# Optimization experiments

Measured on AMD Instinct MI355X. Metric: run time of the kernel, lower is better.

## Reference

```python
import jax, jax.numpy as jnp
import numpy as np

B, T_HIST, D, H = 32768, 50, 3, 512
FUTURE = 30


def gru_cell(x, h, W_ih, W_hh, b_ih, b_hh):
    # PyTorch GRU cell math: gates ordered (r, z, n)
    gi = x @ W_ih.T + b_ih          # [B, 3H]
    gh = h @ W_hh.T + b_hh          # [B, 3H]
    i_r, i_z, i_n = jnp.split(gi, 3, axis=-1)
    h_r, h_z, h_n = jnp.split(gh, 3, axis=-1)
    r = jax.nn.sigmoid(i_r + h_r)
    z = jax.nn.sigmoid(i_z + h_z)
    n = jnp.tanh(i_n + r * h_n)
    return (1.0 - z) * n + z * h


def setup_inputs() -> dict:
    key = jax.random.key(0)
    ks = jax.random.split(key, 20)
    s = 0.04  # ~1/sqrt(H), matches PyTorch uniform init scale
    def p(k, shape):
        return jax.random.normal(k, shape, dtype=jnp.float32) * s
    return {
        "x_input": jax.random.normal(ks[0], (B, T_HIST, D), dtype=jnp.float32),
        "future_len": FUTURE,
        # encoder GRU, layer 0 (input D) and layer 1 (input H)
        "enc_W_ih0": p(ks[1], (3 * H, D)), "enc_W_hh0": p(ks[2], (3 * H, H)),
        "enc_b_ih0": p(ks[3], (3 * H,)),  "enc_b_hh0": p(ks[4], (3 * H,)),
        "enc_W_ih1": p(ks[5], (3 * H, H)), "enc_W_hh1": p(ks[6], (3 * H, H)),
        "enc_b_ih1": p(ks[7], (3 * H,)),  "enc_b_hh1": p(ks[8], (3 * H,)),
        # decoder GRU, layer 0 (input D = output_dim) and layer 1
        "dec_W_ih0": p(ks[9], (3 * H, D)), "dec_W_hh0": p(ks[10], (3 * H, H)),
        "dec_b_ih0": p(ks[11], (3 * H,)), "dec_b_hh0": p(ks[12], (3 * H,)),
        "dec_W_ih1": p(ks[13], (3 * H, H)), "dec_W_hh1": p(ks[14], (3 * H, H)),
        "dec_b_ih1": p(ks[15], (3 * H,)), "dec_b_hh1": p(ks[16], (3 * H,)),
        # output projection
        "fc_W": p(ks[17], (D, H)), "fc_b": p(ks[18], (D,)),
    }


def reference(x_input, future_len,
              enc_W_ih0, enc_W_hh0, enc_b_ih0, enc_b_hh0,
              enc_W_ih1, enc_W_hh1, enc_b_ih1, enc_b_hh1,
              dec_W_ih0, dec_W_hh0, dec_b_ih0, dec_b_hh0,
              dec_W_ih1, dec_W_hh1, dec_b_ih1, dec_b_hh1,
              fc_W, fc_b):
    b = x_input.shape[0]
    h_init = jnp.zeros((b, H), dtype=x_input.dtype)

    # ---- encoder: 2-layer GRU over history (eval mode, no dropout) ----
    def enc_step(carry, x_t):
        h0, h1 = carry
        h0 = gru_cell(x_t, h0, enc_W_ih0, enc_W_hh0, enc_b_ih0, enc_b_hh0)
        h1 = gru_cell(h0, h1, enc_W_ih1, enc_W_hh1, enc_b_ih1, enc_b_hh1)
        return (h0, h1), None

    (h0, h1), _ = jax.lax.scan(enc_step, (h_init, h_init),
                               jnp.swapaxes(x_input, 0, 1))  # [T, B, D]

    def dec_step(carry, _):
        d0, d1, xin = carry
        d0 = gru_cell(xin, d0, dec_W_ih0, dec_W_hh0, dec_b_ih0, dec_b_hh0)
        d1 = gru_cell(d0, d1, dec_W_ih1, dec_W_hh1, dec_b_ih1, dec_b_hh1)
        pred = d1 @ fc_W.T + fc_b  # [B, D]
        return (d0, d1, pred), pred

    _, outs = jax.lax.scan(dec_step, (h0, h1, x_input[:, -1, :]),
                           None, length=future_len)  # [F, B, D]
    return jnp.swapaxes(outs, 0, 1)  # [B, F, D]
```

## Files before the change

kernel.cpp:

```cpp
#include <hip/hip_runtime.h>
#include <hip/hip_fp16.h>
#include <stdint.h>

typedef _Float16 h8 __attribute__((ext_vector_type(8)));
typedef float f4 __attribute__((ext_vector_type(4)));

#define DEV static __device__ __forceinline__

constexpr int BATCH  = 32768;
constexpr int HID    = 512;
constexpr int T_HIST = 50;
constexpr int FUT    = 30;
constexpr int BM = 128, BN = 32, BK = 64;

DEV void gl2lds16(const void* g, void* l) {
  __builtin_amdgcn_global_load_lds(
      (const __attribute__((address_space(1))) void*)g,
      (__attribute__((address_space(3))) void*)l,
      16, 0, 0);
}

DEV float sigm(float x)     { return 1.f / (1.f + __expf(-x)); }
DEV float tanhfast(float x) { return 1.f - 2.f / (__expf(2.f * x) + 1.f); }

__global__ void zero_fill(float4* __restrict__ p, int n4) {
  int i = blockIdx.x * 256 + threadIdx.x;
  if (i < n4) p[i] = float4{0.f, 0.f, 0.f, 0.f};
}

__global__ void pack_w(const float* __restrict__ Wa, const float* __restrict__ Wb,
                       _Float16* __restrict__ out, int KC) {
  int i = blockIdx.x * 256 + threadIdx.x;
  int total = 16 * KC * 3 * 32 * 64;
  if (i >= total) return;
  int k0  = i & 7;
  int k8s = (i >> 3) & 7;
  int n   = (i >> 6) & 31;
  int t   = i >> 11;
  int g   = t % 3;
  int t2  = t / 3;
  int kc  = t2 % KC;
  int nb  = t2 / KC;
  int k8  = k8s ^ (n & 7);
  int row = g * 512 + nb * 32 + n;
  int kg  = kc * 64 + k8 * 8 + k0;
  float v = (kg < 512) ? Wa[(size_t)row * 512 + kg] : Wb[(size_t)row * 512 + kg - 512];
  out[i] = (_Float16)v;
}

__global__ void pack_bias(const float* __restrict__ bih, const float* __restrict__ bhh,
                          float* __restrict__ out) {
  int j = blockIdx.x * 256 + threadIdx.x;
  if (j >= 512) return;
  out[j]        = bih[j]        + bhh[j];
  out[512 + j]  = bih[512 + j]  + bhh[512 + j];
  out[1024 + j] = bih[1024 + j];
  out[1536 + j] = bhh[1024 + j];
}

__global__ void pack_wx(const float* __restrict__ Wih, float* __restrict__ out) {
  int i = blockIdx.x * 256 + threadIdx.x;
  if (i >= 512 * 9) return;
  int j = i / 9, q = i % 9, g = q / 3, k = q % 3;
  out[i] = Wih[(size_t)(g * 512 + j) * 3 + k];
}

template <int KC, bool L0>
__launch_bounds__(256, 3)
__global__ void gru_step(const _Float16* __restrict__ Bp,
                         const _Float16* __restrict__ Alo,
                         const _Float16* __restrict__ Ahi,
                         _Float16* __restrict__ hnew16,
                         const float* __restrict__ bias,
                         const float* __restrict__ Wx,
                         const float* __restrict__ xin,
                         int xstride) {
  __shared__ alignas(16) _Float16 sA[BM * BK];
  __shared__ alignas(16) _Float16 sB[3 * BN * BK];

  const int tid  = threadIdx.x;
  const int wave = tid >> 6;
  const int lane = tid & 63;
  const int quad = lane >> 4;
  const int l15  = lane & 15;
  const int L  = blockIdx.x;
  const int c  = L & 7;
  const int q  = L >> 3;
  const int cb = q & 15;
  const int rb = (c << 5) | (q >> 4);
  const int row0 = rb * BM;
  const int col0 = cb * BN;

  f4 acc_r[2][2]  = {};
  f4 acc_z[2][2]  = {};
  f4 acc_n0[2][2] = {};
  f4 acc_n1[2][2] = {};

  const _Float16* Bblk = Bp + (size_t)cb * KC * (3 * BN * BK);

  for (int kc = 0; kc < KC; ++kc) {
    const _Float16* Asrc = (KC == 16 && kc >= 8) ? Ahi : Alo;
    const int kb = (kc & 7) * BK;
#pragma unroll
    for (int i = 0; i < 4; ++i) {
      int ga = wave * 256 + i * 64 + lane;
      int m = ga >> 3, k8s = ga & 7;
      int k8l = k8s ^ (m & 7);
      gl2lds16(Asrc + (size_t)(row0 + m) * HID + kb + k8l * 8,
               &sA[(wave * 256 + i * 64) * 8]);
    }
    const _Float16* Bsrc = Bblk + (size_t)kc * (3 * BN * BK);
#pragma unroll
    for (int i = 0; i < 3; ++i) {
      int gb = wave * 192 + i * 64 + lane;
      gl2lds16(Bsrc + (size_t)gb * 8, &sB[(wave * 192 + i * 64) * 8]);
    }
    __syncthreads();
#pragma unroll
    for (int s = 0; s < 2; ++s) {
      const int sw = ((s * 4 + quad) ^ (l15 & 7)) * 8;
      h8 af[2];
#pragma unroll
      for (int mt = 0; mt < 2; ++mt)
        af[mt] = *(const h8*)&sA[(wave * 32 + mt * 16 + l15) * BK + sw];
#pragma unroll
      for (int nt = 0; nt < 2; ++nt) {
        const int nrow = nt * 16 + l15;
        h8 br = *(const h8*)&sB[(0 * BN + nrow) * BK + sw];
        h8 bz = *(const h8*)&sB[(1 * BN + nrow) * BK + sw];
        h8 bn = *(const h8*)&sB[(2 * BN + nrow) * BK + sw];
#pragma unroll
        for (int mt = 0; mt < 2; ++mt) {
          acc_r[mt][nt] = __builtin_amdgcn_mfma_f32_16x16x32_f16(af[mt], br, acc_r[mt][nt], 0, 0, 0);
          acc_z[mt][nt] = __builtin_amdgcn_mfma_f32_16x16x32_f16(af[mt], bz, acc_z[mt][nt], 0, 0, 0);
          if (L0 || kc >= 8)
            acc_n1[mt][nt] = __builtin_amdgcn_mfma_f32_16x16x32_f16(af[mt], bn, acc_n1[mt][nt], 0, 0, 0);
          else
            acc_n0[mt][nt] = __builtin_amdgcn_mfma_f32_16x16x32_f16(af[mt], bn, acc_n0[mt][nt], 0, 0, 0);
        }
      }
    }
    __syncthreads();
  }

  const _Float16* hold16 = L0 ? Alo : Ahi;
  float bR[2], bZ[2], bI[2], bH[2];
  float wx[2][9];
#pragma unroll
  for (int nt = 0; nt < 2; ++nt) {
    int j = col0 + nt * 16 + l15;
    bR[nt] = bias[j];
    bZ[nt] = bias[512 + j];
    bI[nt] = bias[1024 + j];
    bH[nt] = bias[1536 + j];
    if constexpr (L0) {
#pragma unroll
      for (int q2 = 0; q2 < 9; ++q2) wx[nt][q2] = Wx[j * 9 + q2];
    }
  }
  float xv[2][4][3];
  if constexpr (L0) {
#pragma unroll
    for (int mt = 0; mt < 2; ++mt)
#pragma unroll
      for (int r = 0; r < 4; ++r) {
        int b = row0 + wave * 32 + mt * 16 + quad * 4 + r;
        const float* xp = xin + (size_t)b * xstride;
        xv[mt][r][0] = xp[0]; xv[mt][r][1] = xp[1]; xv[mt][r][2] = xp[2];
      }
  }
#pragma unroll
  for (int mt = 0; mt < 2; ++mt) {
#pragma unroll
    for (int r = 0; r < 4; ++r) {
      int b = row0 + wave * 32 + mt * 16 + quad * 4 + r;
#pragma unroll
      for (int nt = 0; nt < 2; ++nt) {
        int j = col0 + nt * 16 + l15;
        size_t idx = (size_t)b * HID + j;
        float rr = acc_r[mt][nt][r] + bR[nt];
        float zz = acc_z[mt][nt][r] + bZ[nt];
        float hn = acc_n1[mt][nt][r] + bH[nt];
        float in_;
        if constexpr (L0) {
          const float* w = wx[nt];
          rr += xv[mt][r][0] * w[0] + xv[mt][r][1] * w[1] + xv[mt][r][2] * w[2];
          zz += xv[mt][r][0] * w[3] + xv[mt][r][1] * w[4] + xv[mt][r][2] * w[5];
          in_ = bI[nt] + xv[mt][r][0] * w[6] + xv[mt][r][1] * w[7] + xv[mt][r][2] * w[8];
        } else {
          in_ = acc_n0[mt][nt][r] + bI[nt];
        }
        float rg = sigm(rr);
        float zg = sigm(zz);
        float ng = tanhfast(in_ + rg * hn);
        float hp = (float)hold16[idx];
        float hv = (1.f - zg) * ng + zg * hp;
        hnew16[idx] = (_Float16)hv;
      }
    }
  }
}

__global__ __launch_bounds__(256) void fc_kernel(const _Float16* __restrict__ h,
                                                 const float* __restrict__ W,
                                                 const float* __restrict__ bfc,
                                                 float* __restrict__ out) {
  int wave = threadIdx.x >> 6, lane = threadIdx.x & 63;
  int b = blockIdx.x * 4 + wave;
  const h8* hp = (const h8*)(h + (size_t)b * 512);
  h8 a0 = hp[lane];
  float s[3];
#pragma unroll
  for (int d = 0; d < 3; ++d) {
    const float4* wp = (const float4*)(W + d * 512);
    float4 w0 = wp[lane * 2], w1 = wp[lane * 2 + 1];
    s[d] = (float)a0[0] * w0.x + (float)a0[1] * w0.y + (float)a0[2] * w0.z + (float)a0[3] * w0.w
         + (float)a0[4] * w1.x + (float)a0[5] * w1.y + (float)a0[6] * w1.z + (float)a0[7] * w1.w;
  }
#pragma unroll
  for (int d = 0; d < 3; ++d)
#pragma unroll
    for (int off = 32; off > 0; off >>= 1) s[d] += __shfl_xor(s[d], off, 64);
  if (lane == 0) {
    out[(size_t)b * 90 + 0] = s[0] + bfc[0];
    out[(size_t)b * 90 + 1] = s[1] + bfc[1];
    out[(size_t)b * 90 + 2] = s[2] + bfc[2];
  }
}

extern "C" void kernel_launch(void* const* d_in, const int* in_sizes, int n_in,
                              void* d_out, int out_size, void* d_ws, size_t ws_size,
                              hipStream_t stream) {
  (void)in_sizes; (void)n_in; (void)out_size; (void)ws_size;
  const float* x_input = (const float*)d_in[0];
  const float* eWih0 = (const float*)d_in[2];
  const float* eWhh0 = (const float*)d_in[3];
  const float* ebih0 = (const float*)d_in[4];
  const float* ebhh0 = (const float*)d_in[5];
  const float* eWih1 = (const float*)d_in[6];
  const float* eWhh1 = (const float*)d_in[7];
  const float* ebih1 = (const float*)d_in[8];
  const float* ebhh1 = (const float*)d_in[9];
  const float* dWih0 = (const float*)d_in[10];
  const float* dWhh0 = (const float*)d_in[11];
  const float* dbih0 = (const float*)d_in[12];
  const float* dbhh0 = (const float*)d_in[13];
  const float* dWih1 = (const float*)d_in[14];
  const float* dWhh1 = (const float*)d_in[15];
  const float* dbih1 = (const float*)d_in[16];
  const float* dbhh1 = (const float*)d_in[17];
  const float* fcW   = (const float*)d_in[18];
  const float* fcb   = (const float*)d_in[19];
  float* out = (float*)d_out;

  char* ws = (char*)d_ws;
  const size_t S16 = (size_t)BATCH * HID * 2;
  _Float16* h0h[2] = {(_Float16*)(ws),            (_Float16*)(ws + S16)};
  _Float16* h1h[2] = {(_Float16*)(ws + 2 * S16),  (_Float16*)(ws + 3 * S16)};
  char* p = ws + 4 * S16;
  const size_t W8  = (size_t)16 * 8  * 3 * 32 * 64 * 2;
  const size_t W16 = (size_t)16 * 16 * 3 * 32 * 64 * 2;
  _Float16* pkE0 = (_Float16*)p; p += W8;
  _Float16* pkE1 = (_Float16*)p; p += W16;
  _Float16* pkD0 = (_Float16*)p; p += W8;
  _Float16* pkD1 = (_Float16*)p; p += W16;
  float* bE0 = (float*)p; p += 2048 * 4;
  float* bE1 = (float*)p; p += 2048 * 4;
  float* bD0 = (float*)p; p += 2048 * 4;
  float* bD1 = (float*)p; p += 2048 * 4;
  float* wxE = (float*)p; p += 512 * 9 * 4;
  float* wxD = (float*)p; p += 512 * 9 * 4;

  pack_w<<<dim3(3072), 256, 0, stream>>>(eWhh0, eWhh0, pkE0, 8);
  pack_w<<<dim3(6144), 256, 0, stream>>>(eWih1, eWhh1, pkE1, 16);
  pack_w<<<dim3(3072), 256, 0, stream>>>(dWhh0, dWhh0, pkD0, 8);
  pack_w<<<dim3(6144), 256, 0, stream>>>(dWih1, dWhh1, pkD1, 16);
  pack_bias<<<2, 256, 0, stream>>>(ebih0, ebhh0, bE0);
  pack_bias<<<2, 256, 0, stream>>>(ebih1, ebhh1, bE1);
  pack_bias<<<2, 256, 0, stream>>>(dbih0, dbhh0, bD0);
  pack_bias<<<2, 256, 0, stream>>>(dbih1, dbhh1, bD1);
  pack_wx<<<18, 256, 0, stream>>>(eWih0, wxE);
  pack_wx<<<18, 256, 0, stream>>>(dWih0, wxD);

  {
    int n4 = (int)(S16 / 16);
    zero_fill<<<(n4 + 255) / 256, 256, 0, stream>>>((float4*)h0h[0], n4);
    zero_fill<<<(n4 + 255) / 256, 256, 0, stream>>>((float4*)h1h[0], n4);
  }

  dim3 grid(4096), blk(256);
  int p0 = 0, p1 = 0;
  for (int t = 0; t < T_HIST; ++t) {
    gru_step<8, true><<<grid, blk, 0, stream>>>(pkE0, h0h[p0], nullptr,
                                                h0h[1 - p0], bE0, wxE,
                                                x_input + (size_t)t * 3, 150);
    p0 ^= 1;
    gru_step<16, false><<<grid, blk, 0, stream>>>(pkE1, h0h[p0], h1h[p1],
                                                  h1h[1 - p1], bE1, nullptr, nullptr, 0);
    p1 ^= 1;
  }
  for (int t = 0; t < FUT; ++t) {
    const float* xp; int xs;
    if (t == 0) { xp = x_input + (size_t)49 * 3; xs = 150; }
    else        { xp = out + (size_t)(t - 1) * 3; xs = 90; }
    gru_step<8, true><<<grid, blk, 0, stream>>>(pkD0, h0h[p0], nullptr,
                                                h0h[1 - p0], bD0, wxD, xp, xs);
    p0 ^= 1;
    gru_step<16, false><<<grid, blk, 0, stream>>>(pkD1, h0h[p0], h1h[p1],
                                                  h1h[1 - p1], bD1, nullptr, nullptr, 0);
    p1 ^= 1;
    fc_kernel<<<8192, 256, 0, stream>>>(h1h[p1], fcW, fcb, out + (size_t)t * 3);
  }
}
```

Measured before the change: 15.57 ms.

## Load A fragments directly from global memory and double K chunk size

The activation (A) tile is no longer staged through LDS. Each lane now reads its MFMA fragments straight from global memory into registers. The K chunk grows from 64 to 128, so the weight tile in LDS doubles and the packed weight layout and swizzle are redone for 16 groups of 8 halves. This halves the number of K iterations and barriers and frees the LDS the A tile used, but A reads become uncoalesced 16-byte loads issued inside the MFMA loop with no prefetch.

```diff
diff --git a/kernel.cpp b/kernel.cpp
--- a/kernel.cpp
+++ b/kernel.cpp
@@ -11,7 +11,7 @@
 constexpr int HID    = 512;
 constexpr int T_HIST = 50;
 constexpr int FUT    = 30;
-constexpr int BM = 128, BN = 32, BK = 64;
+constexpr int BM = 128, BN = 32, BK = 128;
 
 DEV void gl2lds16(const void* g, void* l) {
   __builtin_amdgcn_global_load_lds(
@@ -29,21 +29,21 @@
 }
 
 __global__ void pack_w(const float* __restrict__ Wa, const float* __restrict__ Wb,
-                       _Float16* __restrict__ out, int KC) {
+                       _Float16* __restrict__ out, int KCC) {
   int i = blockIdx.x * 256 + threadIdx.x;
-  int total = 16 * KC * 3 * 32 * 64;
+  int total = 16 * KCC * 3 * 32 * 128;
   if (i >= total) return;
-  int k0  = i & 7;
-  int k8s = (i >> 3) & 7;
-  int n   = (i >> 6) & 31;
-  int t   = i >> 11;
-  int g   = t % 3;
-  int t2  = t / 3;
-  int kc  = t2 % KC;
-  int nb  = t2 / KC;
-  int k8  = k8s ^ (n & 7);
-  int row = g * 512 + nb * 32 + n;
-  int kg  = kc * 64 + k8 * 8 + k0;
+  int k0   = i & 7;
+  int g16s = (i >> 3) & 15;
+  int n    = (i >> 7) & 31;
+  int t    = i >> 12;
+  int g    = t % 3;
+  int t2   = t / 3;
+  int kc   = t2 % KCC;
+  int nb   = t2 / KCC;
+  int g16  = g16s ^ (n & 15);
+  int row  = g * 512 + nb * 32 + n;
+  int kg   = kc * 128 + g16 * 8 + k0;
   float v = (kg < 512) ? Wa[(size_t)row * 512 + kg] : Wb[(size_t)row * 512 + kg - 512];
   out[i] = (_Float16)v;
 }
@@ -65,7 +65,7 @@
   out[i] = Wih[(size_t)(g * 512 + j) * 3 + k];
 }
 
-template <int KC, bool L0>
+template <int KCC, bool L0>
 __launch_bounds__(256, 3)
 __global__ void gru_step(const _Float16* __restrict__ Bp,
                          const _Float16* __restrict__ Alo,
@@ -75,7 +75,6 @@
                          const float* __restrict__ Wx,
                          const float* __restrict__ xin,
                          int xstride) {
-  __shared__ alignas(16) _Float16 sA[BM * BK];
   __shared__ alignas(16) _Float16 sB[3 * BN * BK];
 
   const int tid  = threadIdx.x;
@@ -96,44 +95,37 @@
   f4 acc_n0[2][2] = {};
   f4 acc_n1[2][2] = {};
 
-  const _Float16* Bblk = Bp + (size_t)cb * KC * (3 * BN * BK);
-
-  for (int kc = 0; kc < KC; ++kc) {
-    const _Float16* Asrc = (KC == 16 && kc >= 8) ? Ahi : Alo;
-    const int kb = (kc & 7) * BK;
-#pragma unroll
-    for (int i = 0; i < 4; ++i) {
-      int ga = wave * 256 + i * 64 + lane;
-      int m = ga >> 3, k8s = ga & 7;
-      int k8l = k8s ^ (m & 7);
-      gl2lds16(Asrc + (size_t)(row0 + m) * HID + kb + k8l * 8,
-               &sA[(wave * 256 + i * 64) * 8]);
-    }
+  const _Float16* Bblk = Bp + (size_t)cb * KCC * (3 * BN * BK);
+  const size_t aoff0 = (size_t)(row0 + wave * 32 + l15) * HID + quad * 8;
+  const size_t aoff1 = aoff0 + (size_t)16 * HID;
+
+  for (int kc = 0; kc < KCC; ++kc) {
+    const _Float16* Asrc = (KCC == 8 && kc >= 4) ? Ahi : Alo;
+    const int kb = (kc & 3) * BK;
     const _Float16* Bsrc = Bblk + (size_t)kc * (3 * BN * BK);
 #pragma unroll
-    for (int i = 0; i < 3; ++i) {
-      int gb = wave * 192 + i * 64 + lane;
-      gl2lds16(Bsrc + (size_t)gb * 8, &sB[(wave * 192 + i * 64) * 8]);
+    for (int i = 0; i < 6; ++i) {
+      int gb = wave * 384 + i * 64 + lane;
+      gl2lds16(Bsrc + (size_t)gb * 8, &sB[(wave * 384 + i * 64) * 8]);
     }
     __syncthreads();
 #pragma unroll
-    for (int s = 0; s < 2; ++s) {
-      const int sw = ((s * 4 + quad) ^ (l15 & 7)) * 8;
+    for (int s = 0; s < 4; ++s) {
       h8 af[2];
-#pragma unroll
-      for (int mt = 0; mt < 2; ++mt)
-        af[mt] = *(const h8*)&sA[(wave * 32 + mt * 16 + l15) * BK + sw];
+      af[0] = *(const h8*)&Asrc[aoff0 + kb + s * 32];
+      af[1] = *(const h8*)&Asrc[aoff1 + kb + s * 32];
+      const int g16s = (s * 4 + quad) ^ l15;
 #pragma unroll
       for (int nt = 0; nt < 2; ++nt) {
         const int nrow = nt * 16 + l15;
-        h8 br = *(const h8*)&sB[(0 * BN + nrow) * BK + sw];
-        h8 bz = *(const h8*)&sB[(1 * BN + nrow) * BK + sw];
-        h8 bn = *(const h8*)&sB[(2 * BN + nrow) * BK + sw];
+        h8 br = *(const h8*)&sB[((0 * BN + nrow) * 16 + g16s) * 8];
+        h8 bz = *(const h8*)&sB[((1 * BN + nrow) * 16 + g16s) * 8];
+        h8 bn = *(const h8*)&sB[((2 * BN + nrow) * 16 + g16s) * 8];
 #pragma unroll
         for (int mt = 0; mt < 2; ++mt) {
           acc_r[mt][nt] = __builtin_amdgcn_mfma_f32_16x16x32_f16(af[mt], br, acc_r[mt][nt], 0, 0, 0);
           acc_z[mt][nt] = __builtin_amdgcn_mfma_f32_16x16x32_f16(af[mt], bz, acc_z[mt][nt], 0, 0, 0);
-          if (L0 || kc >= 8)
+          if (L0 || kc >= 4)
             acc_n1[mt][nt] = __builtin_amdgcn_mfma_f32_16x16x32_f16(af[mt], bn, acc_n1[mt][nt], 0, 0, 0);
           else
             acc_n0[mt][nt] = __builtin_amdgcn_mfma_f32_16x16x32_f16(af[mt], bn, acc_n0[mt][nt], 0, 0, 0);
@@ -258,12 +250,12 @@
   _Float16* h0h[2] = {(_Float16*)(ws),            (_Float16*)(ws + S16)};
   _Float16* h1h[2] = {(_Float16*)(ws + 2 * S16),  (_Float16*)(ws + 3 * S16)};
   char* p = ws + 4 * S16;
-  const size_t W8  = (size_t)16 * 8  * 3 * 32 * 64 * 2;
-  const size_t W16 = (size_t)16 * 16 * 3 * 32 * 64 * 2;
-  _Float16* pkE0 = (_Float16*)p; p += W8;
-  _Float16* pkE1 = (_Float16*)p; p += W16;
-  _Float16* pkD0 = (_Float16*)p; p += W8;
-  _Float16* pkD1 = (_Float16*)p; p += W16;
+  const size_t W4 = (size_t)16 * 4 * 3 * 32 * 128 * 2;
+  const size_t W8 = (size_t)16 * 8 * 3 * 32 * 128 * 2;
+  _Float16* pkE0 = (_Float16*)p; p += W4;
+  _Float16* pkE1 = (_Float16*)p; p += W8;
+  _Float16* pkD0 = (_Float16*)p; p += W4;
+  _Float16* pkD1 = (_Float16*)p; p += W8;
   float* bE0 = (float*)p; p += 2048 * 4;
   float* bE1 = (float*)p; p += 2048 * 4;
   float* bD0 = (float*)p; p += 2048 * 4;
@@ -271,10 +263,10 @@
   float* wxE = (float*)p; p += 512 * 9 * 4;
   float* wxD = (float*)p; p += 512 * 9 * 4;
 
-  pack_w<<<dim3(3072), 256, 0, stream>>>(eWhh0, eWhh0, pkE0, 8);
-  pack_w<<<dim3(6144), 256, 0, stream>>>(eWih1, eWhh1, pkE1, 16);
-  pack_w<<<dim3(3072), 256, 0, stream>>>(dWhh0, dWhh0, pkD0, 8);
-  pack_w<<<dim3(6144), 256, 0, stream>>>(dWih1, dWhh1, pkD1, 16);
+  pack_w<<<dim3(3072), 256, 0, stream>>>(eWhh0, eWhh0, pkE0, 4);
+  pack_w<<<dim3(6144), 256, 0, stream>>>(eWih1, eWhh1, pkE1, 8);
+  pack_w<<<dim3(3072), 256, 0, stream>>>(dWhh0, dWhh0, pkD0, 4);
+  pack_w<<<dim3(6144), 256, 0, stream>>>(dWih1, dWhh1, pkD1, 8);
   pack_bias<<<2, 256, 0, stream>>>(ebih0, ebhh0, bE0);
   pack_bias<<<2, 256, 0, stream>>>(ebih1, ebhh1, bE1);
   pack_bias<<<2, 256, 0, stream>>>(dbih0, dbhh0, bD0);
@@ -291,23 +283,23 @@
   dim3 grid(4096), blk(256);
   int p0 = 0, p1 = 0;
   for (int t = 0; t < T_HIST; ++t) {
-    gru_step<8, true><<<grid, blk, 0, stream>>>(pkE0, h0h[p0], nullptr,
+    gru_step<4, true><<<grid, blk, 0, stream>>>(pkE0, h0h[p0], nullptr,
                                                 h0h[1 - p0], bE0, wxE,
                                                 x_input + (size_t)t * 3, 150);
     p0 ^= 1;
-    gru_step<16, false><<<grid, blk, 0, stream>>>(pkE1, h0h[p0], h1h[p1],
-                                                  h1h[1 - p1], bE1, nullptr, nullptr, 0);
+    gru_step<8, false><<<grid, blk, 0, stream>>>(pkE1, h0h[p0], h1h[p1],
+                                                 h1h[1 - p1], bE1, nullptr, nullptr, 0);
     p1 ^= 1;
   }
   for (int t = 0; t < FUT; ++t) {
     const float* xp; int xs;
     if (t == 0) { xp = x_input + (size_t)49 * 3; xs = 150; }
     else        { xp = out + (size_t)(t - 1) * 3; xs = 90; }
-    gru_step<8, true><<<grid, blk, 0, stream>>>(pkD0, h0h[p0], nullptr,
+    gru_step<4, true><<<grid, blk, 0, stream>>>(pkD0, h0h[p0], nullptr,
                                                 h0h[1 - p0], bD0, wxD, xp, xs);
     p0 ^= 1;
-    gru_step<16, false><<<grid, blk, 0, stream>>>(pkD1, h0h[p0], h1h[p1],
-                                                  h1h[1 - p1], bD1, nullptr, nullptr, 0);
+    gru_step<8, false><<<grid, blk, 0, stream>>>(pkD1, h0h[p0], h1h[p1],
+                                                 h1h[1 - p1], bD1, nullptr, nullptr, 0);
     p1 ^= 1;
     fc_kernel<<<8192, 256, 0, stream>>>(h1h[p1], fcW, fcb, out + (size_t)t * 3);
   }
```

Result: slower. 20.97 ms (+34.6%).

## Double GRU GEMM row tile and spill split n-gate accumulator to LDS

Applied to the files above, without the earlier changes.

Raises the block row tile from 128 to 256, halving the grid and giving each wave four M sub-tiles, so each loaded weight tile is reused across twice as many batch rows. To keep register pressure manageable, the separate input-side n-gate accumulator is replaced by a single accumulator whose first-half result is stashed to a 32 KB LDS buffer at the K midpoint. The costs are higher LDS use and lower occupancy (launch bounds go from 3 to 2 blocks), plus a larger epilogue per thread.

```diff
diff --git a/kernel.cpp b/kernel.cpp
--- a/kernel.cpp
+++ b/kernel.cpp
@@ -11,7 +11,7 @@
 constexpr int HID    = 512;
 constexpr int T_HIST = 50;
 constexpr int FUT    = 30;
-constexpr int BM = 128, BN = 32, BK = 64;
+constexpr int BM = 256, BN = 32, BK = 64;
 
 DEV void gl2lds16(const void* g, void* l) {
   __builtin_amdgcn_global_load_lds(
@@ -66,7 +66,7 @@
 }
 
 template <int KC, bool L0>
-__launch_bounds__(256, 3)
+__launch_bounds__(256, 2)
 __global__ void gru_step(const _Float16* __restrict__ Bp,
                          const _Float16* __restrict__ Alo,
                          const _Float16* __restrict__ Ahi,
@@ -77,6 +77,7 @@
                          int xstride) {
   __shared__ alignas(16) _Float16 sA[BM * BK];
   __shared__ alignas(16) _Float16 sB[3 * BN * BK];
+  __shared__ float sN[L0 ? 64 : 32 * 256];
 
   const int tid  = threadIdx.x;
   const int wave = tid >> 6;
@@ -87,27 +88,39 @@
   const int c  = L & 7;
   const int q  = L >> 3;
   const int cb = q & 15;
-  const int rb = (c << 5) | (q >> 4);
+  const int rb = (c << 4) | (q >> 4);
   const int row0 = rb * BM;
   const int col0 = cb * BN;
 
-  f4 acc_r[2][2]  = {};
-  f4 acc_z[2][2]  = {};
-  f4 acc_n0[2][2] = {};
-  f4 acc_n1[2][2] = {};
+  f4 acc_r[4][2] = {};
+  f4 acc_z[4][2] = {};
+  f4 acc_n[4][2] = {};
 
   const _Float16* Bblk = Bp + (size_t)cb * KC * (3 * BN * BK);
 
   for (int kc = 0; kc < KC; ++kc) {
     const _Float16* Asrc = (KC == 16 && kc >= 8) ? Ahi : Alo;
     const int kb = (kc & 7) * BK;
-#pragma unroll
-    for (int i = 0; i < 4; ++i) {
-      int ga = wave * 256 + i * 64 + lane;
+    if constexpr (!L0) {
+      if (kc == 8) {
+#pragma unroll
+        for (int mt = 0; mt < 4; ++mt)
+#pragma unroll
+          for (int nt = 0; nt < 2; ++nt)
+#pragma unroll
+            for (int r = 0; r < 4; ++r) {
+              sN[((mt * 2 + nt) * 4 + r) * 256 + tid] = acc_n[mt][nt][r];
+              acc_n[mt][nt][r] = 0.f;
+            }
+      }
+    }
+#pragma unroll
+    for (int i = 0; i < 8; ++i) {
+      int ga = wave * 512 + i * 64 + lane;
       int m = ga >> 3, k8s = ga & 7;
       int k8l = k8s ^ (m & 7);
       gl2lds16(Asrc + (size_t)(row0 + m) * HID + kb + k8l * 8,
-               &sA[(wave * 256 + i * 64) * 8]);
+               &sA[(wave * 512 + i * 64) * 8]);
     }
     const _Float16* Bsrc = Bblk + (size_t)kc * (3 * BN * BK);
 #pragma unroll
@@ -119,10 +132,10 @@
 #pragma unroll
     for (int s = 0; s < 2; ++s) {
       const int sw = ((s * 4 + quad) ^ (l15 & 7)) * 8;
-      h8 af[2];
-#pragma unroll
-      for (int mt = 0; mt < 2; ++mt)
-        af[mt] = *(const h8*)&sA[(wave * 32 + mt * 16 + l15) * BK + sw];
+      h8 af[4];
+#pragma unroll
+      for (int mt = 0; mt < 4; ++mt)
+        af[mt] = *(const h8*)&sA[(wave * 64 + mt * 16 + l15) * BK + sw];
 #pragma unroll
       for (int nt = 0; nt < 2; ++nt) {
         const int nrow = nt * 16 + l15;
@@ -130,13 +143,10 @@
         h8 bz = *(const h8*)&sB[(1 * BN + nrow) * BK + sw];
         h8 bn = *(const h8*)&sB[(2 * BN + nrow) * BK + sw];
 #pragma unroll
-        for (int mt = 0; mt < 2; ++mt) {
+        for (int mt = 0; mt < 4; ++mt) {
           acc_r[mt][nt] = __builtin_amdgcn_mfma_f32_16x16x32_f16(af[mt], br, acc_r[mt][nt], 0, 0, 0);
           acc_z[mt][nt] = __builtin_amdgcn_mfma_f32_16x16x32_f16(af[mt], bz, acc_z[mt][nt], 0, 0, 0);
-          if (L0 || kc >= 8)
-            acc_n1[mt][nt] = __builtin_amdgcn_mfma_f32_16x16x32_f16(af[mt], bn, acc_n1[mt][nt], 0, 0, 0);
-          else
-            acc_n0[mt][nt] = __builtin_amdgcn_mfma_f32_16x16x32_f16(af[mt], bn, acc_n0[mt][nt], 0, 0, 0);
+          acc_n[mt][nt] = __builtin_amdgcn_mfma_f32_16x16x32_f16(af[mt], bn, acc_n[mt][nt], 0, 0, 0);
         }
       }
     }
@@ -158,37 +168,35 @@
       for (int q2 = 0; q2 < 9; ++q2) wx[nt][q2] = Wx[j * 9 + q2];
     }
   }
-  float xv[2][4][3];
-  if constexpr (L0) {
-#pragma unroll
-    for (int mt = 0; mt < 2; ++mt)
+#pragma unroll
+  for (int mt = 0; mt < 4; ++mt) {
+    float xv[4][3];
+    if constexpr (L0) {
 #pragma unroll
       for (int r = 0; r < 4; ++r) {
-        int b = row0 + wave * 32 + mt * 16 + quad * 4 + r;
+        int b = row0 + wave * 64 + mt * 16 + quad * 4 + r;
         const float* xp = xin + (size_t)b * xstride;
-        xv[mt][r][0] = xp[0]; xv[mt][r][1] = xp[1]; xv[mt][r][2] = xp[2];
+        xv[r][0] = xp[0]; xv[r][1] = xp[1]; xv[r][2] = xp[2];
       }
-  }
-#pragma unroll
-  for (int mt = 0; mt < 2; ++mt) {
+    }
 #pragma unroll
     for (int r = 0; r < 4; ++r) {
-      int b = row0 + wave * 32 + mt * 16 + quad * 4 + r;
+      int b = row0 + wave * 64 + mt * 16 + quad * 4 + r;
 #pragma unroll
       for (int nt = 0; nt < 2; ++nt) {
         int j = col0 + nt * 16 + l15;
         size_t idx = (size_t)b * HID + j;
         float rr = acc_r[mt][nt][r] + bR[nt];
         float zz = acc_z[mt][nt][r] + bZ[nt];
-        float hn = acc_n1[mt][nt][r] + bH[nt];
+        float hn = acc_n[mt][nt][r] + bH[nt];
         float in_;
         if constexpr (L0) {
           const float* w = wx[nt];
-          rr += xv[mt][r][0] * w[0] + xv[mt][r][1] * w[1] + xv[mt][r][2] * w[2];
-          zz += xv[mt][r][0] * w[3] + xv[mt][r][1] * w[4] + xv[mt][r][2] * w[5];
-          in_ = bI[nt] + xv[mt][r][0] * w[6] + xv[mt][r][1] * w[7] + xv[mt][r][2] * w[8];
+          rr += xv[r][0] * w[0] + xv[r][1] * w[1] + xv[r][2] * w[2];
+          zz += xv[r][0] * w[3] + xv[r][1] * w[4] + xv[r][2] * w[5];
+          in_ = bI[nt] + xv[r][0] * w[6] + xv[r][1] * w[7] + xv[r][2] * w[8];
         } else {
-          in_ = acc_n0[mt][nt][r] + bI[nt];
+          in_ = sN[((mt * 2 + nt) * 4 + r) * 256 + tid] + bI[nt];
         }
         float rg = sigm(rr);
         float zg = sigm(zz);
@@ -288,7 +296,7 @@
     zero_fill<<<(n4 + 255) / 256, 256, 0, stream>>>((float4*)h1h[0], n4);
   }
 
-  dim3 grid(4096), blk(256);
+  dim3 grid(2048), blk(256);
   int p0 = 0, p1 = 0;
   for (int t = 0; t < T_HIST; ++t) {
     gru_step<8, true><<<grid, blk, 0, stream>>>(pkE0, h0h[p0], nullptr,
```

New measurement: 15.90 ms. 1.02x slower.

## Double-buffer LDS tiles to overlap global loads with MFMA compute

Applied to the files above, without the earlier changes.

Splits the shared-memory A and B tiles into two buffers so that each K-chunk's global-to-LDS loads are issued into the other buffer while the current chunk is multiplied. This removes one barrier per iteration and hides load latency behind MFMA work. Address offsets are now precomputed once per thread. In exchange LDS use per block doubles, so launch bounds drop from 3 to 2 blocks per CU, which lowers occupancy.

```diff
diff --git a/kernel.cpp b/kernel.cpp
--- a/kernel.cpp
+++ b/kernel.cpp
@@ -66,7 +66,7 @@
 }
 
 template <int KC, bool L0>
-__launch_bounds__(256, 3)
+__launch_bounds__(256, 2)
 __global__ void gru_step(const _Float16* __restrict__ Bp,
                          const _Float16* __restrict__ Alo,
                          const _Float16* __restrict__ Ahi,
@@ -75,8 +75,8 @@
                          const float* __restrict__ Wx,
                          const float* __restrict__ xin,
                          int xstride) {
-  __shared__ alignas(16) _Float16 sA[BM * BK];
-  __shared__ alignas(16) _Float16 sB[3 * BN * BK];
+  __shared__ alignas(16) _Float16 sA[2][BM * BK];
+  __shared__ alignas(16) _Float16 sB[2][3 * BN * BK];
 
   const int tid  = threadIdx.x;
   const int wave = tid >> 6;
@@ -96,39 +96,50 @@
   f4 acc_n0[2][2] = {};
   f4 acc_n1[2][2] = {};
 
-  const _Float16* Bblk = Bp + (size_t)cb * KC * (3 * BN * BK);
-
+  int aoffs[4];
+#pragma unroll
+  for (int i = 0; i < 4; ++i) {
+    int ga = wave * 256 + i * 64 + lane;
+    int m = ga >> 3, k8s = ga & 7;
+    aoffs[i] = m * HID + (k8s ^ (m & 7)) * 8;
+  }
+  int boffs[3];
+#pragma unroll
+  for (int i = 0; i < 3; ++i) boffs[i] = (wave * 192 + i * 64 + lane) * 8;
+
+  const _Float16* Abase0 = Alo + (size_t)row0 * HID;
+  const _Float16* Abase1 = (KC == 16) ? Ahi + (size_t)row0 * HID : nullptr;
+  const _Float16* Bbase  = Bp + (size_t)cb * KC * (3 * BN * BK);
+
+  auto stage = [&](int kc, int buf) {
+    const _Float16* ab = ((KC == 16 && kc >= 8) ? Abase1 : Abase0) + (kc & 7) * BK;
+    const _Float16* bb = Bbase + (size_t)kc * (3 * BN * BK);
+#pragma unroll
+    for (int i = 0; i < 4; ++i)
+      gl2lds16(ab + aoffs[i], &sA[buf][(wave * 256 + i * 64) * 8]);
+#pragma unroll
+    for (int i = 0; i < 3; ++i)
+      gl2lds16(bb + boffs[i], &sB[buf][(wave * 192 + i * 64) * 8]);
+  };
+
+  stage(0, 0);
   for (int kc = 0; kc < KC; ++kc) {
-    const _Float16* Asrc = (KC == 16 && kc >= 8) ? Ahi : Alo;
-    const int kb = (kc & 7) * BK;
-#pragma unroll
-    for (int i = 0; i < 4; ++i) {
-      int ga = wave * 256 + i * 64 + lane;
-      int m = ga >> 3, k8s = ga & 7;
-      int k8l = k8s ^ (m & 7);
-      gl2lds16(Asrc + (size_t)(row0 + m) * HID + kb + k8l * 8,
-               &sA[(wave * 256 + i * 64) * 8]);
-    }
-    const _Float16* Bsrc = Bblk + (size_t)kc * (3 * BN * BK);
-#pragma unroll
-    for (int i = 0; i < 3; ++i) {
-      int gb = wave * 192 + i * 64 + lane;
-      gl2lds16(Bsrc + (size_t)gb * 8, &sB[(wave * 192 + i * 64) * 8]);
-    }
+    const int cur = kc & 1;
     __syncthreads();
+    if (kc + 1 < KC) stage(kc + 1, 1 - cur);
 #pragma unroll
     for (int s = 0; s < 2; ++s) {
       const int sw = ((s * 4 + quad) ^ (l15 & 7)) * 8;
       h8 af[2];
 #pragma unroll
       for (int mt = 0; mt < 2; ++mt)
-        af[mt] = *(const h8*)&sA[(wave * 32 + mt * 16 + l15) * BK + sw];
+        af[mt] = *(const h8*)&sA[cur][(wave * 32 + mt * 16 + l15) * BK + sw];
 #pragma unroll
       for (int nt = 0; nt < 2; ++nt) {
         const int nrow = nt * 16 + l15;
-        h8 br = *(const h8*)&sB[(0 * BN + nrow) * BK + sw];
-        h8 bz = *(const h8*)&sB[(1 * BN + nrow) * BK + sw];
-        h8 bn = *(const h8*)&sB[(2 * BN + nrow) * BK + sw];
+        h8 br = *(const h8*)&sB[cur][(0 * BN + nrow) * BK + sw];
+        h8 bz = *(const h8*)&sB[cur][(1 * BN + nrow) * BK + sw];
+        h8 bn = *(const h8*)&sB[cur][(2 * BN + nrow) * BK + sw];
 #pragma unroll
         for (int mt = 0; mt < 2; ++mt) {
           acc_r[mt][nt] = __builtin_amdgcn_mfma_f32_16x16x32_f16(af[mt], br, acc_r[mt][nt], 0, 0, 0);
@@ -140,7 +151,6 @@
         }
       }
     }
-    __syncthreads();
   }
 
   const _Float16* hold16 = L0 ? Alo : Ahi;
```

New measurement: 18.95 ms. 1.22x slower.
